# Performance work log

Hardware: AMD Instinct MI355X
Metric: run time of the kernel (lower is better)

## Reference

```python
import jax, jax.numpy as jnp
import numpy as np

D = 10          # tree depth (perfect binary tree, heap layout)
K = 2           # MAX_CHILD
N = 2 ** D - 1  # nodes per tree = 1023
LD = 256        # latent_dim
B = 128         # batch of trees


def setup_inputs() -> dict:
    key = jax.random.key(0)
    ks = jax.random.split(key, 24)
    p = lambda k, shape: (jax.random.normal(k, shape, jnp.float32) * 0.05)
    return {
        "x_embed": jax.random.normal(ks[0], (B, N, LD), jnp.float32),
        "init_embedding": jax.random.normal(ks[1], (B, LD), jnp.float32),
        # leaf gates cx, ox
        "Wcx": p(ks[2], (LD, LD)), "bcx": p(ks[3], (LD,)),
        "Wox": p(ks[4], (LD, LD)), "box": p(ks[5], (LD,)),
        # token-input gates ix, fx, ux
        "Wix": p(ks[6], (LD, LD)), "bix": p(ks[7], (LD,)),
        "Wfx": p(ks[8], (LD, LD)), "bfx": p(ks[9], (LD,)),
        "Wux": p(ks[10], (LD, LD)), "bux": p(ks[11], (LD,)),
        # per-child gates: i_gates[K], f_gates[K][K], u_gates[K]
        "Wi": p(ks[12], (K, LD, LD)), "bi": p(ks[13], (K, LD)),
        "Wf": p(ks[14], (K, K, LD, LD)), "bf": p(ks[15], (K, K, LD)),
        "Wu": p(ks[16], (K, LD, LD)), "bu": p(ks[17], (K, LD)),
        # output projection oend: Linear(3*latent_dim, latent_dim)
        "Woend": p(ks[18], (3 * LD, LD)), "boend": p(ks[19], (LD,)),
    }


def _tree_lstm(x_embed, Wcx, bcx, Wox, box, Wix, bix, Wfx, bfx, Wux, bux,
               Wi, bi, Wf, bf, Wu, bu):
    lin = lambda x, W, b: x @ W + b
    # --- leaves (deepest level): c = cx(x); h = sigmoid(ox(x)) * tanh(c) ---
    leaf_start = 2 ** (D - 1) - 1
    x_leaf = x_embed[:, leaf_start:]                       # [B, 2^(D-1), d]
    c_leaf = lin(x_leaf, Wcx, bcx)
    h_leaf = jax.nn.sigmoid(lin(x_leaf, Wox, box)) * jnp.tanh(c_leaf)
    c_all = jnp.zeros_like(x_embed).at[:, leaf_start:].set(c_leaf)
    h_all = jnp.zeros_like(x_embed).at[:, leaf_start:].set(h_leaf)
    # --- internal levels, bottom-up (fixed D-1 iterations, vectorized over B*width) ---
    for lvl in range(D - 2, -1, -1):
        s, e = 2 ** lvl - 1, 2 ** (lvl + 1) - 1
        idx = np.arange(s, e)
        ch = np.stack([2 * idx + 1, 2 * idx + 2], axis=1)  # [w, K] heap children
        hch = h_all[:, ch]                                 # [B, w, K, d]
        cch = c_all[:, ch]                                 # [B, w, K, d]
        x = x_embed[:, s:e]                                # [B, w, d]
        # i = sigmoid(ix(x) + sum_k i_gates[k](h_k))
        i = jax.nn.sigmoid(lin(x, Wix, bix)
                           + jnp.einsum('bwkd,kde->bwe', hch, Wi) + bi.sum(0))
        # f_vals[k] = fx(x) + sum_j f_gates[k][j](h_j)   (NO sigmoid, faithful to source)
        f = (lin(x, Wfx, bfx)[:, :, None, :]
             + jnp.einsum('bwjd,kjde->bwke', hch, Wf) + bf.sum(1))   # [B, w, K, d]
        # u = tanh(ux(x) + sum_k u_gates[k](h_k))
        u = jnp.tanh(lin(x, Wux, bux)
                     + jnp.einsum('bwkd,kde->bwe', hch, Wu) + bu.sum(0))
        c = i * u + jnp.sum(f * cch, axis=2)
        h = jnp.tanh(c)
        c_all = c_all.at[:, s:e].set(c)
        h_all = h_all.at[:, s:e].set(h)
    return c_all[:, 0], h_all[:, 0]                        # root state (c, h)


def reference(x_embed, init_embedding, Wcx, bcx, Wox, box, Wix, bix, Wfx, bfx,
              Wux, bux, Wi, bi, Wf, bf, Wu, bu, Woend, boend):
    c_root, h_root = _tree_lstm(x_embed, Wcx, bcx, Wox, box, Wix, bix,
                                Wfx, bfx, Wux, bux, Wi, bi, Wf, bf, Wu, bu)
    s = jnp.concatenate([init_embedding, c_root, h_root], axis=1)  # [B, 3d]
    return jnp.tanh(s @ Woend + boend)                             # [B, d]
```

## Files before the change

kernel.cpp:

```cpp
#include <hip/hip_runtime.h>
#include <hip/hip_bf16.h>
#include <math.h>


#define NNODES 1023
#define BATCH  128
#define LDIM   256

typedef __attribute__((ext_vector_type(8))) short short8;
typedef __attribute__((ext_vector_type(4))) float f32x4;

__device__ __forceinline__ float sigmoidf_(float x) {
    return 1.f / (1.f + expf(-x));
}

__device__ __forceinline__ void split3(float x, ushort& h, ushort& m, ushort& l) {
    unsigned u = __float_as_uint(x);
    unsigned hu = (u + 0x7FFFu + ((u >> 16) & 1u)) & 0xFFFF0000u;
    h = (ushort)(hu >> 16);
    float r = x - __uint_as_float(hu);
    unsigned ur = __float_as_uint(r);
    unsigned mu = (ur + 0x7FFFu + ((ur >> 16) & 1u)) & 0xFFFF0000u;
    m = (ushort)(mu >> 16);
    float r2 = r - __uint_as_float(mu);
    unsigned u2 = __float_as_uint(r2);
    l = (ushort)((u2 + 0x7FFFu + ((u2 >> 16) & 1u)) >> 16);
}

__device__ __forceinline__ unsigned cvt_pk_bf16(float lo, float hi) {
    unsigned r;
    asm("v_cvt_pk_bf16_f32 %0, %1, %2" : "=v"(r) : "v"(lo), "v"(hi));
    return r;
}

struct P3 { unsigned h, m, l; };
__device__ __forceinline__ P3 pack2v(float x0, float x1) {
    P3 p;
    p.h = cvt_pk_bf16(x0, x1);
    float h0 = __uint_as_float(p.h << 16);
    float h1 = __uint_as_float(p.h & 0xFFFF0000u);
    float r0 = x0 - h0, r1 = x1 - h1;
    p.m = cvt_pk_bf16(r0, r1);
    float m0 = __uint_as_float(p.m << 16);
    float m1 = __uint_as_float(p.m & 0xFFFF0000u);
    p.l = cvt_pk_bf16(r0 - m0, r1 - m1);
    return p;
}

struct VF { short8 h, m, l; };
__device__ __forceinline__ VF split8(float4 a, float4 b) {
    P3 p0 = pack2v(a.x, a.y), p1 = pack2v(a.z, a.w);
    P3 p2 = pack2v(b.x, b.y), p3 = pack2v(b.z, b.w);
    VF r;
    r.h = __builtin_bit_cast(short8, make_uint4(p0.h, p1.h, p2.h, p3.h));
    r.m = __builtin_bit_cast(short8, make_uint4(p0.m, p1.m, p2.m, p3.m));
    r.l = __builtin_bit_cast(short8, make_uint4(p0.l, p1.l, p2.l, p3.l));
    return r;
}

__global__ __launch_bounds__(256) void build_weights(
    const float* __restrict__ Wix, const float* __restrict__ bix,
    const float* __restrict__ Wfx, const float* __restrict__ bfx,
    const float* __restrict__ Wux, const float* __restrict__ bux,
    const float* __restrict__ Wi,  const float* __restrict__ bi,
    const float* __restrict__ Wf,  const float* __restrict__ bf,
    const float* __restrict__ Wu,  const float* __restrict__ bu,
    const float* __restrict__ Wcx, const float* __restrict__ bcx,
    const float* __restrict__ Wox, const float* __restrict__ box,
    float* __restrict__ Wbig, float* __restrict__ bias_big,
    float* __restrict__ Wleaf, float* __restrict__ bias_leaf)
{
    int i = blockIdx.x * blockDim.x + threadIdx.x;
    if (i < 768 * 1024) {
        int k = i >> 10, n = i & 1023;
        int g = n >> 8, nn = n & 255;
        float v;
        if (g == 0) {
            v = (k < 256) ? Wix[k * 256 + nn]
              : (k < 512) ? Wi[(k - 256) * 256 + nn]
                          : Wi[65536 + (k - 512) * 256 + nn];
        } else if (g == 1) {
            v = (k < 256) ? Wux[k * 256 + nn]
              : (k < 512) ? Wu[(k - 256) * 256 + nn]
                          : Wu[65536 + (k - 512) * 256 + nn];
        } else {
            int kf = g - 2;
            v = (k < 256) ? Wfx[k * 256 + nn]
              : (k < 512) ? Wf[((kf * 2 + 0) * 256 + (k - 256)) * 256 + nn]
                          : Wf[((kf * 2 + 1) * 256 + (k - 512)) * 256 + nn];
        }
        Wbig[i] = v;
        return;
    }
    i -= 768 * 1024;
    if (i < 1024) {
        int g = i >> 8, nn = i & 255;
        float v;
        if (g == 0)      v = bix[nn] + bi[nn] + bi[256 + nn];
        else if (g == 1) v = bux[nn] + bu[nn] + bu[256 + nn];
        else if (g == 2) v = bfx[nn] + bf[nn] + bf[256 + nn];
        else             v = bfx[nn] + bf[512 + nn] + bf[768 + nn];
        bias_big[i] = v;
        return;
    }
    i -= 1024;
    if (i < 256 * 512) {
        int k = i >> 9, n = i & 511;
        Wleaf[i] = (n < 256) ? Wcx[k * 256 + n] : Wox[k * 256 + (n - 256)];
        return;
    }
    i -= 256 * 512;
    if (i < 512) {
        bias_leaf[i] = (i < 256) ? bcx[i] : box[i - 256];
    }
}

__global__ __launch_bounds__(256) void split_weights_T(
    const float* __restrict__ Wbig,
    ushort* __restrict__ Wth, ushort* __restrict__ Wtm, ushort* __restrict__ Wtl)
{
    __shared__ float sh[32][33];
    const int k0 = blockIdx.x * 32, n0 = blockIdx.y * 32;
    const int t = threadIdx.x;
    {
        int r = t >> 3, c4 = (t & 7) * 4;
        float4 v = *(const float4*)&Wbig[(size_t)(k0 + r) * 1024 + n0 + c4];
        sh[r][c4] = v.x; sh[r][c4 + 1] = v.y; sh[r][c4 + 2] = v.z; sh[r][c4 + 3] = v.w;
    }
    __syncthreads();
    int n = t >> 3, kc = (t & 7) * 4;
    ushort oh[4], om[4], ol[4];
#pragma unroll
    for (int j = 0; j < 4; ++j)
        split3(sh[kc + j][n], oh[j], om[j], ol[j]);
    size_t o = (size_t)(n0 + n) * 768 + k0 + kc;
    *(ushort4*)&Wth[o] = make_ushort4(oh[0], oh[1], oh[2], oh[3]);
    *(ushort4*)&Wtm[o] = make_ushort4(om[0], om[1], om[2], om[3]);
    *(ushort4*)&Wtl[o] = make_ushort4(ol[0], ol[1], ol[2], ol[3]);
}

__global__ __launch_bounds__(256) void split_wleaf_T(
    const float* __restrict__ Wleaf,
    ushort* __restrict__ Lth, ushort* __restrict__ Ltm, ushort* __restrict__ Ltl)
{
    __shared__ float sh[32][33];
    const int k0 = blockIdx.x * 32, n0 = blockIdx.y * 32;
    const int t = threadIdx.x;
    {
        int r = t >> 3, c4 = (t & 7) * 4;
        float4 v = *(const float4*)&Wleaf[(size_t)(k0 + r) * 512 + n0 + c4];
        sh[r][c4] = v.x; sh[r][c4 + 1] = v.y; sh[r][c4 + 2] = v.z; sh[r][c4 + 3] = v.w;
    }
    __syncthreads();
    int n = t >> 3, kc = (t & 7) * 4;
    ushort oh[4], om[4], ol[4];
#pragma unroll
    for (int j = 0; j < 4; ++j)
        split3(sh[kc + j][n], oh[j], om[j], ol[j]);
    size_t o = (size_t)(n0 + n) * 256 + k0 + kc;
    *(ushort4*)&Lth[o] = make_ushort4(oh[0], oh[1], oh[2], oh[3]);
    *(ushort4*)&Ltm[o] = make_ushort4(om[0], om[1], om[2], om[3]);
    *(ushort4*)&Ltl[o] = make_ushort4(ol[0], ol[1], ol[2], ol[3]);
}

__global__ __launch_bounds__(256, 3) void mfma_level_pack(
    const float* __restrict__ x_embed,
    const float* __restrict__ hChild, const float* __restrict__ cChild,
    const ushort* __restrict__ Wth, const ushort* __restrict__ Wtm,
    const ushort* __restrict__ Wtl,
    const float* __restrict__ bias,
    float* __restrict__ hOut, float* __restrict__ cOut, int nstart)
{
    constexpr int AST = 40;
    __shared__ __align__(16) ushort Wlds[3][128 * AST];

    const int tid  = threadIdx.x;
    const int node = blockIdx.x;
    const int gy   = blockIdx.y;
    const int lane = tid & 63, wid = tid >> 6;
    const int srow = tid & 127, shalf = tid >> 7;

    const size_t nb = (size_t)(((srow >> 5) << 8) + gy * 32 + (srow & 31)) * 768;
    const ushort* w0 = Wth + nb;
    const ushort* w1 = Wtm + nb;
    const ushort* w2 = Wtl + nb;

    const int b0 = wid * 32 + (lane & 15);
    const int b1 = b0 + 16;
    const int kl = (lane >> 4) * 8;
    const float* x0p = x_embed + ((size_t)b0 * NNODES + (nstart + node)) * LDIM + kl;
    const float* x1p = x_embed + ((size_t)b1 * NNODES + (nstart + node)) * LDIM + kl;
    const float* l0p = hChild + ((size_t)(2 * node) * BATCH + b0) * LDIM + kl;
    const float* l1p = hChild + ((size_t)(2 * node) * BATCH + b1) * LDIM + kl;
    const size_t RSTEP = (size_t)BATCH * LDIM;

    f32x4 acc[8][2];
#pragma unroll
    for (int ct = 0; ct < 8; ++ct)
#pragma unroll
        for (int t2 = 0; t2 < 2; ++t2) acc[ct][t2] = (f32x4){0.f, 0.f, 0.f, 0.f};

    float4 v00, v01, v10, v11;
    int4 w00, w01, w10, w11, w20, w21;

#define TREE_LOADS(IT)                                                         \
    {                                                                          \
        const int seg_  = (IT) >> 3;                                           \
        const int koff_ = ((IT) & 7) * 32;                                     \
        const float* pa0_ = (seg_ == 0) ? x0p : (seg_ == 1) ? l0p : (l0p + RSTEP); \
        const float* pa1_ = (seg_ == 0) ? x1p : (seg_ == 1) ? l1p : (l1p + RSTEP); \
        pa0_ += koff_; pa1_ += koff_;                                          \
        v00 = *(const float4*)(pa0_);                                          \
        v01 = *(const float4*)(pa0_ + 4);                                      \
        v10 = *(const float4*)(pa1_);                                          \
        v11 = *(const float4*)(pa1_ + 4);                                      \
        const int bko_ = (IT) * 32 + shalf * 16;                               \
        w00 = *(const int4*)(w0 + bko_); w01 = *(const int4*)(w0 + bko_ + 8);  \
        w10 = *(const int4*)(w1 + bko_); w11 = *(const int4*)(w1 + bko_ + 8);  \
        w20 = *(const int4*)(w2 + bko_); w21 = *(const int4*)(w2 + bko_ + 8);  \
    }

    TREE_LOADS(0);
    for (int it = 0; it < 24; ++it) {
        if (it) __syncthreads();
        {
            const int base = srow * AST + shalf * 16;
            *(int4*)&Wlds[0][base]     = w00;
            *(int4*)&Wlds[0][base + 8] = w01;
            *(int4*)&Wlds[1][base]     = w10;
            *(int4*)&Wlds[1][base + 8] = w11;
            *(int4*)&Wlds[2][base]     = w20;
            *(int4*)&Wlds[2][base + 8] = w21;
        }
        __syncthreads();
        VF f0 = split8(v00, v01);
        VF f1 = split8(v10, v11);
        if (it + 1 < 24) TREE_LOADS(it + 1);
#pragma unroll
        for (int ct = 0; ct < 8; ++ct) {
            const int cb = (ct * 16 + (lane & 15)) * AST + (lane >> 4) * 8;
            short8 wh = *(const short8*)&Wlds[0][cb];
            short8 wm = *(const short8*)&Wlds[1][cb];
            short8 wl = *(const short8*)&Wlds[2][cb];
            acc[ct][0] = __builtin_amdgcn_mfma_f32_16x16x32_bf16(wl, f0.h, acc[ct][0], 0, 0, 0);
            acc[ct][1] = __builtin_amdgcn_mfma_f32_16x16x32_bf16(wl, f1.h, acc[ct][1], 0, 0, 0);
            acc[ct][0] = __builtin_amdgcn_mfma_f32_16x16x32_bf16(wh, f0.l, acc[ct][0], 0, 0, 0);
            acc[ct][1] = __builtin_amdgcn_mfma_f32_16x16x32_bf16(wh, f1.l, acc[ct][1], 0, 0, 0);
            acc[ct][0] = __builtin_amdgcn_mfma_f32_16x16x32_bf16(wm, f0.m, acc[ct][0], 0, 0, 0);
            acc[ct][1] = __builtin_amdgcn_mfma_f32_16x16x32_bf16(wm, f1.m, acc[ct][1], 0, 0, 0);
            acc[ct][0] = __builtin_amdgcn_mfma_f32_16x16x32_bf16(wm, f0.h, acc[ct][0], 0, 0, 0);
            acc[ct][1] = __builtin_amdgcn_mfma_f32_16x16x32_bf16(wm, f1.h, acc[ct][1], 0, 0, 0);
            acc[ct][0] = __builtin_amdgcn_mfma_f32_16x16x32_bf16(wh, f0.m, acc[ct][0], 0, 0, 0);
            acc[ct][1] = __builtin_amdgcn_mfma_f32_16x16x32_bf16(wh, f1.m, acc[ct][1], 0, 0, 0);
            acc[ct][0] = __builtin_amdgcn_mfma_f32_16x16x32_bf16(wh, f0.h, acc[ct][0], 0, 0, 0);
            acc[ct][1] = __builtin_amdgcn_mfma_f32_16x16x32_bf16(wh, f1.h, acc[ct][1], 0, 0, 0);
        }
    }
#undef TREE_LOADS

    const size_t cLb = (size_t)(2 * node) * BATCH * LDIM;
    const size_t cRb = cLb + (size_t)BATCH * LDIM;
    const size_t ob  = (size_t)node * BATCH * LDIM;
#pragma unroll
    for (int half = 0; half < 2; ++half) {
        const int nc = gy * 32 + half * 16 + ((lane >> 4) << 2);
        const float4 bi4 = *(const float4*)&bias[nc];
        const float4 bu4 = *(const float4*)&bias[256 + nc];
        const float4 b04 = *(const float4*)&bias[512 + nc];
        const float4 b14 = *(const float4*)&bias[768 + nc];
        const float bi_[4] = {bi4.x, bi4.y, bi4.z, bi4.w};
        const float bu_[4] = {bu4.x, bu4.y, bu4.z, bu4.w};
        const float b0_[4] = {b04.x, b04.y, b04.z, b04.w};
        const float b1_[4] = {b14.x, b14.y, b14.z, b14.w};
#pragma unroll
        for (int Nt = 0; Nt < 2; ++Nt) {
            const int b = wid * 32 + Nt * 16 + (lane & 15);
            float4 cL = *(const float4*)&cChild[cLb + (size_t)b * LDIM + nc];
            float4 cR = *(const float4*)&cChild[cRb + (size_t)b * LDIM + nc];
            float cl4[4] = {cL.x, cL.y, cL.z, cL.w};
            float cr4[4] = {cR.x, cR.y, cR.z, cR.w};
            float4 c4, h4;
            float* cp = (float*)&c4; float* hp = (float*)&h4;
#pragma unroll
            for (int j = 0; j < 4; ++j) {
                float gi = sigmoidf_(acc[0 + half][Nt][j] + bi_[j]);
                float gu = tanhf(acc[2 + half][Nt][j] + bu_[j]);
                float f0 = acc[4 + half][Nt][j] + b0_[j];
                float f1 = acc[6 + half][Nt][j] + b1_[j];
                float c  = gi * gu + f0 * cl4[j] + f1 * cr4[j];
                cp[j] = c;
                hp[j] = tanhf(c);
            }
            *(float4*)&cOut[ob + (size_t)b * LDIM + nc] = c4;
            *(float4*)&hOut[ob + (size_t)b * LDIM + nc] = h4;
        }
    }
}

__global__ __launch_bounds__(256, 3) void leaf_mfma(
    const float* __restrict__ x_embed,
    const ushort* __restrict__ Lth, const ushort* __restrict__ Ltm,
    const ushort* __restrict__ Ltl,
    const float* __restrict__ bias_leaf,
    float* __restrict__ hOut, float* __restrict__ cOut)
{
    constexpr int AST = 40;
    __shared__ __align__(16) ushort Wlds[3][64 * AST];
    __shared__ __align__(16) ushort Vlds[3][128 * AST];

    const int tid = threadIdx.x;
    const int ln  = blockIdx.x;
    const int gy  = blockIdx.y;
    const int lane = tid & 63, wid = tid >> 6;
    const int ni = wid & 1, bw = wid >> 1;
    const int srow = tid & 127, shalf = tid >> 7;
    const int wrow = tid & 63, whalf = (tid >> 6) & 1;

    const float* aX = x_embed + ((size_t)srow * NNODES + (511 + ln)) * LDIM;
    const size_t nbw = (size_t)(((wrow >> 5) << 8) + gy * 32 + (wrow & 31)) * 256;
    const ushort* l0 = Lth + nbw;
    const ushort* l1 = Ltm + nbw;
    const ushort* l2 = Ltl + nbw;

    f32x4 acc[2][4];
#pragma unroll
    for (int g = 0; g < 2; ++g)
#pragma unroll
        for (int t2 = 0; t2 < 4; ++t2) acc[g][t2] = (f32x4){0.f, 0.f, 0.f, 0.f};

    float4 a0, a1, a2, a3;
    int4 w00, w01, w10, w11, w20, w21;

#define LEAF_LOADS(IT)                                                         \
    {                                                                          \
        const float* ap_ = aX + (IT) * 32 + shalf * 16;                        \
        a0 = *(const float4*)(ap_);                                            \
        a1 = *(const float4*)(ap_ + 4);                                        \
        a2 = *(const float4*)(ap_ + 8);                                        \
        a3 = *(const float4*)(ap_ + 12);                                       \
        if (tid < 128) {                                                       \
            const int bko_ = (IT) * 32 + whalf * 16;                           \
            w00 = *(const int4*)(l0 + bko_); w01 = *(const int4*)(l0 + bko_ + 8); \
            w10 = *(const int4*)(l1 + bko_); w11 = *(const int4*)(l1 + bko_ + 8); \
            w20 = *(const int4*)(l2 + bko_); w21 = *(const int4*)(l2 + bko_ + 8); \
        }                                                                      \
    }

    LEAF_LOADS(0);
    for (int it = 0; it < 8; ++it) {
        if (it) __syncthreads();
        {
            P3 p0 = pack2v(a0.x, a0.y), p1 = pack2v(a0.z, a0.w);
            P3 p2 = pack2v(a1.x, a1.y), p3 = pack2v(a1.z, a1.w);
            P3 p4 = pack2v(a2.x, a2.y), p5 = pack2v(a2.z, a2.w);
            P3 p6 = pack2v(a3.x, a3.y), p7 = pack2v(a3.z, a3.w);
            const int base = srow * AST + shalf * 16;
            *(int4*)&Vlds[0][base]     = make_int4((int)p0.h, (int)p1.h, (int)p2.h, (int)p3.h);
            *(int4*)&Vlds[0][base + 8] = make_int4((int)p4.h, (int)p5.h, (int)p6.h, (int)p7.h);
            *(int4*)&Vlds[1][base]     = make_int4((int)p0.m, (int)p1.m, (int)p2.m, (int)p3.m);
            *(int4*)&Vlds[1][base + 8] = make_int4((int)p4.m, (int)p5.m, (int)p6.m, (int)p7.m);
            *(int4*)&Vlds[2][base]     = make_int4((int)p0.l, (int)p1.l, (int)p2.l, (int)p3.l);
            *(int4*)&Vlds[2][base + 8] = make_int4((int)p4.l, (int)p5.l, (int)p6.l, (int)p7.l);
            if (tid < 128) {
                const int bw_ = wrow * AST + whalf * 16;
                *(int4*)&Wlds[0][bw_]     = w00;
                *(int4*)&Wlds[0][bw_ + 8] = w01;
                *(int4*)&Wlds[1][bw_]     = w10;
                *(int4*)&Wlds[1][bw_ + 8] = w11;
                *(int4*)&Wlds[2][bw_]     = w20;
                *(int4*)&Wlds[2][bw_ + 8] = w21;
            }
        }
        __syncthreads();
        if (it + 1 < 8) LEAF_LOADS(it + 1);
        {
            short8 vf[4][3];
#pragma unroll
            for (int Nt = 0; Nt < 4; ++Nt) {
                const int rb = (bw * 64 + Nt * 16 + (lane & 15)) * AST + (lane >> 4) * 8;
#pragma unroll
                for (int s = 0; s < 3; ++s) vf[Nt][s] = *(const short8*)&Vlds[s][rb];
            }
#pragma unroll
            for (int g = 0; g < 2; ++g) {
                const int cb = (g * 32 + ni * 16 + (lane & 15)) * AST + (lane >> 4) * 8;
                short8 wh = *(const short8*)&Wlds[0][cb];
                short8 wm = *(const short8*)&Wlds[1][cb];
                short8 wl = *(const short8*)&Wlds[2][cb];
#pragma unroll
                for (int Nt = 0; Nt < 4; ++Nt)
                    acc[g][Nt] = __builtin_amdgcn_mfma_f32_16x16x32_bf16(wl, vf[Nt][0], acc[g][Nt], 0, 0, 0);
#pragma unroll
                for (int Nt = 0; Nt < 4; ++Nt)
                    acc[g][Nt] = __builtin_amdgcn_mfma_f32_16x16x32_bf16(wh, vf[Nt][2], acc[g][Nt], 0, 0, 0);
#pragma unroll
                for (int Nt = 0; Nt < 4; ++Nt)
                    acc[g][Nt] = __builtin_amdgcn_mfma_f32_16x16x32_bf16(wm, vf[Nt][1], acc[g][Nt], 0, 0, 0);
#pragma unroll
                for (int Nt = 0; Nt < 4; ++Nt)
                    acc[g][Nt] = __builtin_amdgcn_mfma_f32_16x16x32_bf16(wm, vf[Nt][0], acc[g][Nt], 0, 0, 0);
#pragma unroll
                for (int Nt = 0; Nt < 4; ++Nt)
                    acc[g][Nt] = __builtin_amdgcn_mfma_f32_16x16x32_bf16(wh, vf[Nt][1], acc[g][Nt], 0, 0, 0);
#pragma unroll
                for (int Nt = 0; Nt < 4; ++Nt)
                    acc[g][Nt] = __builtin_amdgcn_mfma_f32_16x16x32_bf16(wh, vf[Nt][0], acc[g][Nt], 0, 0, 0);
            }
        }
    }
#undef LEAF_LOADS

    const int nc = gy * 32 + ni * 16 + ((lane >> 4) << 2);
    const size_t ob = (size_t)ln * BATCH * LDIM;
    const float4 bc4 = *(const float4*)&bias_leaf[nc];
    const float4 bo4 = *(const float4*)&bias_leaf[256 + nc];
    const float bc_[4] = {bc4.x, bc4.y, bc4.z, bc4.w};
    const float bo_[4] = {bo4.x, bo4.y, bo4.z, bo4.w};
#pragma unroll
    for (int Nt = 0; Nt < 4; ++Nt) {
        const int b = bw * 64 + Nt * 16 + (lane & 15);
        float4 c4, h4;
        float* cp = (float*)&c4; float* hp = (float*)&h4;
#pragma unroll
        for (int j = 0; j < 4; ++j) {
            float c = acc[0][Nt][j] + bc_[j];
            float o = acc[1][Nt][j] + bo_[j];
            cp[j] = c;
            hp[j] = sigmoidf_(o) * tanhf(c);
        }
        size_t po = ob + (size_t)b * LDIM + nc;
        *(float4*)&cOut[po] = c4;
        *(float4*)&hOut[po] = h4;
    }
}

__global__ __launch_bounds__(256) void leaf_kernel(
    const float* __restrict__ x_embed,
    const float* __restrict__ Wleaf, const float* __restrict__ bias_leaf,
    float* __restrict__ hOut, float* __restrict__ cOut)
{
    __shared__ float As[16 * 68];
    __shared__ float Bs[2 * 16 * 64];
    float acc[2][4][4] = {};
    const int tid = threadIdx.x;
    const int ty = tid >> 4, tx = tid & 15;
    const int row0 = blockIdx.x * 64;
    const int n0 = blockIdx.y * 64;
    const int w = row0 >> 7;
    const int ar = tid >> 2;
    const int kq = (tid & 3) * 4;
    const int b = (row0 + ar) & 127;
    const float* xrow = x_embed + ((size_t)b * NNODES + 511 + w) * LDIM;

    for (int k0 = 0; k0 < 256; k0 += 16) {
        float4 av = *(const float4*)(xrow + k0 + kq);
        As[(kq + 0) * 68 + ar] = av.x;
        As[(kq + 1) * 68 + ar] = av.y;
        As[(kq + 2) * 68 + ar] = av.z;
        As[(kq + 3) * 68 + ar] = av.w;
#pragma unroll
        for (int q = 0; q < 2; ++q) {
            int L = q * 256 + tid;
            int g = L >> 8, kk = (L >> 4) & 15, n4 = (L & 15) * 4;
            float4 bv = *(const float4*)(Wleaf + (size_t)(k0 + kk) * 512 + g * 256 + n0 + n4);
            *(float4*)&Bs[(g * 16 + kk) * 64 + n4] = bv;
        }
        __syncthreads();
#pragma unroll
        for (int kk = 0; kk < 16; ++kk) {
            float4 a = *(const float4*)&As[kk * 68 + ty * 4];
            float av4[4] = {a.x, a.y, a.z, a.w};
#pragma unroll
            for (int g = 0; g < 2; ++g) {
                float4 bb = *(const float4*)&Bs[(g * 16 + kk) * 64 + tx * 4];
                float bv4[4] = {bb.x, bb.y, bb.z, bb.w};
#pragma unroll
                for (int ii = 0; ii < 4; ++ii)
#pragma unroll
                    for (int jj = 0; jj < 4; ++jj)
                        acc[g][ii][jj] += av4[ii] * bv4[jj];
            }
        }
        __syncthreads();
    }
#pragma unroll
    for (int ii = 0; ii < 4; ++ii) {
        int r = row0 + ty * 4 + ii;
        int nc = n0 + tx * 4;
        float4 c4, h4;
        float* cp = (float*)&c4; float* hp = (float*)&h4;
#pragma unroll
        for (int jj = 0; jj < 4; ++jj) {
            int n = nc + jj;
            float ac = acc[0][ii][jj] + bias_leaf[n];
            float ao = acc[1][ii][jj] + bias_leaf[256 + n];
            cp[jj] = ac;
            hp[jj] = sigmoidf_(ao) * tanhf(ac);
        }
        *(float4*)&cOut[(size_t)r * LDIM + nc] = c4;
        *(float4*)&hOut[(size_t)r * LDIM + nc] = h4;
    }
}

__global__ __launch_bounds__(256) void level_kernel(
    const float* __restrict__ x_embed,
    const float* __restrict__ hChild, const float* __restrict__ cChild,
    const float* __restrict__ Wbig, const float* __restrict__ bias_big,
    float* __restrict__ hOut, float* __restrict__ cOut,
    int nstart)
{
    __shared__ float As[16 * 68];
    __shared__ float Bs[4 * 16 * 64];
    float acc[4][4][4] = {};
    const int tid = threadIdx.x;
    const int ty = tid >> 4, tx = tid & 15;
    const int row0 = blockIdx.x * 64;
    const int n0 = blockIdx.y * 64;
    const int w = row0 >> 7;
    const int ar = tid >> 2;
    const int kq = (tid & 3) * 4;
    const int b = (row0 + ar) & 127;
    const float* srcX = x_embed + ((size_t)b * NNODES + nstart + w) * LDIM;
    const float* srcL = hChild + ((size_t)(2 * w) * BATCH + b) * LDIM;
    const float* srcR = hChild + ((size_t)(2 * w + 1) * BATCH + b) * LDIM;

    for (int k0 = 0; k0 < 768; k0 += 16) {
        int seg = k0 >> 8, off = k0 & 255;
        const float* src = (seg == 0) ? srcX : (seg == 1) ? srcL : srcR;
        float4 av = *(const float4*)(src + off + kq);
        As[(kq + 0) * 68 + ar] = av.x;
        As[(kq + 1) * 68 + ar] = av.y;
        As[(kq + 2) * 68 + ar] = av.z;
        As[(kq + 3) * 68 + ar] = av.w;
#pragma unroll
        for (int q = 0; q < 4; ++q) {
            int L = q * 256 + tid;
            int g = L >> 8, kk = (L >> 4) & 15, n4 = (L & 15) * 4;
            float4 bv = *(const float4*)(Wbig + (size_t)(k0 + kk) * 1024 + g * 256 + n0 + n4);
            *(float4*)&Bs[(g * 16 + kk) * 64 + n4] = bv;
        }
        __syncthreads();
#pragma unroll
        for (int kk = 0; kk < 16; ++kk) {
            float4 a = *(const float4*)&As[kk * 68 + ty * 4];
            float av4[4] = {a.x, a.y, a.z, a.w};
#pragma unroll
            for (int g = 0; g < 4; ++g) {
                float4 bb = *(const float4*)&Bs[(g * 16 + kk) * 64 + tx * 4];
                float bv4[4] = {bb.x, bb.y, bb.z, bb.w};
#pragma unroll
                for (int ii = 0; ii < 4; ++ii)
#pragma unroll
                    for (int jj = 0; jj < 4; ++jj)
                        acc[g][ii][jj] += av4[ii] * bv4[jj];
            }
        }
        __syncthreads();
    }
    const size_t cLbase = ((size_t)(2 * w) * BATCH) * LDIM;
    const size_t cRbase = ((size_t)(2 * w + 1) * BATCH) * LDIM;
#pragma unroll
    for (int ii = 0; ii < 4; ++ii) {
        int r = row0 + ty * 4 + ii;
        int bb2 = r & 127;
        int nc = n0 + tx * 4;
        float4 cL = *(const float4*)&cChild[cLbase + (size_t)bb2 * LDIM + nc];
        float4 cR = *(const float4*)&cChild[cRbase + (size_t)bb2 * LDIM + nc];
        float cl4[4] = {cL.x, cL.y, cL.z, cL.w};
        float cr4[4] = {cR.x, cR.y, cR.z, cR.w};
        float4 c4, h4;
        float* cp = (float*)&c4; float* hp = (float*)&h4;
#pragma unroll
        for (int jj = 0; jj < 4; ++jj) {
            int n = nc + jj;
            float gi = sigmoidf_(acc[0][ii][jj] + bias_big[n]);
            float gu = tanhf(acc[1][ii][jj] + bias_big[256 + n]);
            float f0 = acc[2][ii][jj] + bias_big[512 + n];
            float f1 = acc[3][ii][jj] + bias_big[768 + n];
            float c = gi * gu + f0 * cl4[jj] + f1 * cr4[jj];
            cp[jj] = c;
            hp[jj] = tanhf(c);
        }
        *(float4*)&cOut[(size_t)r * LDIM + nc] = c4;
        *(float4*)&hOut[(size_t)r * LDIM + nc] = h4;
    }
}

__global__ __launch_bounds__(256) void gemm_part4(
    const float* __restrict__ x_embed, const float* __restrict__ hChild,
    const float* __restrict__ Wbig,
    float* __restrict__ part, int nstart, int rowsTotal)
{
    __shared__ float As[16 * 68];
    __shared__ float Bs[4 * 16 * 64];
    float acc[4][4][4] = {};
    const int tid = threadIdx.x;
    const int ty = tid >> 4, tx = tid & 15;
    const int row0 = blockIdx.x * 64;
    const int n0 = blockIdx.y * 64;
    const int seg = blockIdx.z;
    const int w = row0 >> 7;
    const int ar = tid >> 2;
    const int kq = (tid & 3) * 4;
    const int b = (row0 + ar) & 127;
    const float* src =
        (seg == 0) ? x_embed + ((size_t)b * NNODES + nstart + w) * LDIM
                   : hChild + ((size_t)(2 * w + (seg - 1)) * BATCH + b) * LDIM;

    for (int k0 = 0; k0 < 256; k0 += 16) {
        float4 av = *(const float4*)(src + k0 + kq);
        As[(kq + 0) * 68 + ar] = av.x;
        As[(kq + 1) * 68 + ar] = av.y;
        As[(kq + 2) * 68 + ar] = av.z;
        As[(kq + 3) * 68 + ar] = av.w;
#pragma unroll
        for (int q = 0; q < 4; ++q) {
            int L = q * 256 + tid;
            int g = L >> 8, kk = (L >> 4) & 15, n4 = (L & 15) * 4;
            float4 bv = *(const float4*)(Wbig + (size_t)(seg * 256 + k0 + kk) * 1024
                                         + g * 256 + n0 + n4);
            *(float4*)&Bs[(g * 16 + kk) * 64 + n4] = bv;
        }
        __syncthreads();
#pragma unroll
        for (int kk = 0; kk < 16; ++kk) {
            float4 a = *(const float4*)&As[kk * 68 + ty * 4];
            float av4[4] = {a.x, a.y, a.z, a.w};
#pragma unroll
            for (int g = 0; g < 4; ++g) {
                float4 bb = *(const float4*)&Bs[(g * 16 + kk) * 64 + tx * 4];
                float bv4[4] = {bb.x, bb.y, bb.z, bb.w};
#pragma unroll
                for (int ii = 0; ii < 4; ++ii)
#pragma unroll
                    for (int jj = 0; jj < 4; ++jj)
                        acc[g][ii][jj] += av4[ii] * bv4[jj];
            }
        }
        __syncthreads();
    }
#pragma unroll
    for (int ii = 0; ii < 4; ++ii) {
        int r = row0 + ty * 4 + ii;
        size_t base = ((size_t)seg * rowsTotal + r) * 1024 + n0 + tx * 4;
#pragma unroll
        for (int g = 0; g < 4; ++g)
            *(float4*)&part[base + g * 256] = *(float4*)acc[g][ii];
    }
}

__global__ __launch_bounds__(256) void combine_eps(
    const float* __restrict__ part, const float* __restrict__ cChild,
    const float* __restrict__ bias,
    float* __restrict__ hOut, float* __restrict__ cOut, int rowsTotal)
{
    int idx = blockIdx.x * 256 + threadIdx.x;
    int row = idx >> 6, n = (idx & 63) * 4;
    size_t sseg = (size_t)rowsTotal * 1024;
    const float* p0 = part + (size_t)row * 1024 + n;
    float s[4][4];
#pragma unroll
    for (int g = 0; g < 4; ++g) {
        float4 a = *(const float4*)(p0 + g * 256);
        float4 b = *(const float4*)(p0 + sseg + g * 256);
        float4 c = *(const float4*)(p0 + 2 * sseg + g * 256);
        s[g][0] = a.x + b.x + c.x; s[g][1] = a.y + b.y + c.y;
        s[g][2] = a.z + b.z + c.z; s[g][3] = a.w + b.w + c.w;
    }
    int node = row >> 7, b = row & 127;
    float4 cL = *(const float4*)&cChild[((size_t)(2 * node) * BATCH + b) * LDIM + n];
    float4 cR = *(const float4*)&cChild[((size_t)(2 * node + 1) * BATCH + b) * LDIM + n];
    float cl4[4] = {cL.x, cL.y, cL.z, cL.w};
    float cr4[4] = {cR.x, cR.y, cR.z, cR.w};
    float4 c4, h4;
    float* cp = (float*)&c4; float* hp = (float*)&h4;
#pragma unroll
    for (int jj = 0; jj < 4; ++jj) {
        int nn = n + jj;
        float gi = sigmoidf_(s[0][jj] + bias[nn]);
        float gu = tanhf(s[1][jj] + bias[256 + nn]);
        float f0 = s[2][jj] + bias[512 + nn];
        float f1 = s[3][jj] + bias[768 + nn];
        float c = gi * gu + f0 * cl4[jj] + f1 * cr4[jj];
        cp[jj] = c;
        hp[jj] = tanhf(c);
    }
    *(float4*)&cOut[(size_t)row * LDIM + n] = c4;
    *(float4*)&hOut[(size_t)row * LDIM + n] = h4;
}

__global__ __launch_bounds__(256) void final_kernel(
    const float* __restrict__ init_emb,
    const float* __restrict__ cRoot, const float* __restrict__ hRoot,
    const float* __restrict__ Woend, const float* __restrict__ boend,
    float* __restrict__ out)
{
    __shared__ float sv[768];
    int b = blockIdx.x, t = threadIdx.x;
    sv[t]       = init_emb[(size_t)b * 256 + t];
    sv[256 + t] = cRoot[(size_t)b * 256 + t];
    sv[512 + t] = hRoot[(size_t)b * 256 + t];
    __syncthreads();
    float acc = boend[t];
#pragma unroll 4
    for (int d = 0; d < 768; ++d)
        acc += sv[d] * Woend[(size_t)d * 256 + t];
    out[(size_t)b * 256 + t] = tanhf(acc);
}

extern "C" void kernel_launch(void* const* d_in, const int* in_sizes, int n_in,
                              void* d_out, int out_size, void* d_ws, size_t ws_size,
                              hipStream_t stream)
{
    const float* x_embed  = (const float*)d_in[0];
    const float* init_emb = (const float*)d_in[1];
    const float* Wcx = (const float*)d_in[2];  const float* bcx = (const float*)d_in[3];
    const float* Wox = (const float*)d_in[4];  const float* box = (const float*)d_in[5];
    const float* Wix = (const float*)d_in[6];  const float* bix = (const float*)d_in[7];
    const float* Wfx = (const float*)d_in[8];  const float* bfx = (const float*)d_in[9];
    const float* Wux = (const float*)d_in[10]; const float* bux = (const float*)d_in[11];
    const float* Wi  = (const float*)d_in[12]; const float* bi  = (const float*)d_in[13];
    const float* Wf  = (const float*)d_in[14]; const float* bf  = (const float*)d_in[15];
    const float* Wu  = (const float*)d_in[16]; const float* bu  = (const float*)d_in[17];
    const float* Woend = (const float*)d_in[18]; const float* boend = (const float*)d_in[19];
    float* out = (float*)d_out;
    float* ws  = (float*)d_ws;

    size_t off = 0;
    float* hA = ws + off; off += (size_t)512 * 128 * 256;
    float* cA = ws + off; off += (size_t)512 * 128 * 256;
    float* hB = ws + off; off += (size_t)256 * 128 * 256;
    float* cB = ws + off; off += (size_t)256 * 128 * 256;
    float* Wbig      = ws + off; off += (size_t)768 * 1024;
    float* bias_big  = ws + off; off += 1024;
    float* Wleaf     = ws + off; off += (size_t)256 * 512;
    float* bias_leaf = ws + off; off += 512;
    ushort* Wth = (ushort*)(ws + off); off += (size_t)768 * 1024 / 2;
    ushort* Wtm = (ushort*)(ws + off); off += (size_t)768 * 1024 / 2;
    ushort* Wtl = (ushort*)(ws + off); off += (size_t)768 * 1024 / 2;
    ushort* Lth = (ushort*)(ws + off); off += (size_t)512 * 256 / 2;
    ushort* Ltm = (ushort*)(ws + off); off += (size_t)512 * 256 / 2;
    ushort* Ltl = (ushort*)(ws + off); off += (size_t)512 * 256 / 2;
    size_t mfma_need = off * sizeof(float);
    size_t part_off = off;
    float* part = ws + part_off;

    bool mfma_ok = mfma_need <= ws_size;

    {
        int total = 768 * 1024 + 1024 + 256 * 512 + 512;
        int blocks = (total + 255) / 256;
        build_weights<<<blocks, 256, 0, stream>>>(
            Wix, bix, Wfx, bfx, Wux, bux, Wi, bi, Wf, bf, Wu, bu,
            Wcx, bcx, Wox, box, Wbig, bias_big, Wleaf, bias_leaf);
    }
    if (mfma_ok) {
        split_weights_T<<<dim3(24, 32), 256, 0, stream>>>(Wbig, Wth, Wtm, Wtl);
        split_wleaf_T<<<dim3(8, 16), 256, 0, stream>>>(Wleaf, Lth, Ltm, Ltl);
    }

    if (mfma_ok) {
        leaf_mfma<<<dim3(512, 8), 256, 0, stream>>>(
            x_embed, Lth, Ltm, Ltl, bias_leaf, hA, cA);
    } else {
        leaf_kernel<<<dim3(1024, 4), 256, 0, stream>>>(
            x_embed, Wleaf, bias_leaf, hA, cA);
    }

    float* hbufs[2] = {hA, hB};
    float* cbufs[2] = {cA, cB};
    int child = 0;
    for (int lvl = 8; lvl >= 0; --lvl) {
        int W = 1 << lvl, s = W - 1;
        int outb = child ^ 1;
        size_t rows = (size_t)W * 128;
        bool split = (W <= 16) &&
                     ((part_off + 3 * rows * 1024) * sizeof(float) <= ws_size);
        if (lvl >= 5 && mfma_ok) {
            mfma_level_pack<<<dim3(W, 8), 256, 0, stream>>>(
                x_embed, hbufs[child], cbufs[child], Wth, Wtm, Wtl, bias_big,
                hbufs[outb], cbufs[outb], s);
        } else if (split) {
            gemm_part4<<<dim3(W * 2, 4, 3), 256, 0, stream>>>(
                x_embed, hbufs[child], Wbig, part, s, (int)rows);
            combine_eps<<<(int)(rows / 4), 256, 0, stream>>>(
                part, cbufs[child], bias_big, hbufs[outb], cbufs[outb], (int)rows);
        } else {
            level_kernel<<<dim3(W * 2, 4), 256, 0, stream>>>(
                x_embed, hbufs[child], cbufs[child], Wbig, bias_big,
                hbufs[outb], cbufs[outb], s);
        }
        child = outb;
    }

    final_kernel<<<128, 256, 0, stream>>>(init_emb, cbufs[child], hbufs[child],
                                          Woend, boend, out);
}
```

Baseline: 1.080 ms.

## Double-buffer weight tiles in LDS with conflict-free layout and MFMA priority

Weight tiles for the level kernel now go into two LDS buffers, so the next tile's store overlaps the current MFMA loop. This cuts the two barriers per iteration to one. Global weight loads are issued two iterations ahead, and the LDS layout is reorganised to a k-chunk-major form with no padding. s_setprio is raised around the MFMA block. The cost is more LDS per block (48KB vs 30KB), which may reduce occupancy below the launch-bounds target of 3 blocks, plus more live registers from the deeper prefetch.

Measured after the change: 1.064 ms (median of 2 runs). Within noise of the previous version (-1.4%).

```diff
diff --git a/kernel.cpp b/kernel.cpp
--- a/kernel.cpp
+++ b/kernel.cpp
@@ -171,8 +171,7 @@
     const float* __restrict__ bias,
     float* __restrict__ hOut, float* __restrict__ cOut, int nstart)
 {
-    constexpr int AST = 40;
-    __shared__ __align__(16) ushort Wlds[3][128 * AST];
+    __shared__ __align__(16) ushort Wlds[2][12288];
 
     const int tid  = threadIdx.x;
     const int node = blockIdx.x;
@@ -194,6 +193,9 @@
     const float* l1p = hChild + ((size_t)(2 * node) * BATCH + b1) * LDIM + kl;
     const size_t RSTEP = (size_t)BATCH * LDIM;
 
+    const int wbase = 2 * shalf * 1024 + srow * 8;
+    const int rbase = (lane >> 4) * 1024 + (lane & 15) * 8;
+
     f32x4 acc[8][2];
 #pragma unroll
     for (int ct = 0; ct < 8; ++ct)
@@ -203,7 +205,14 @@
     float4 v00, v01, v10, v11;
     int4 w00, w01, w10, w11, w20, w21;
 
-#define TREE_LOADS(IT)                                                         \
+#define W_LOADS(IT)                                                            \
+    {                                                                          \
+        const int bko_ = (IT) * 32 + shalf * 16;                               \
+        w00 = *(const int4*)(w0 + bko_); w01 = *(const int4*)(w0 + bko_ + 8);  \
+        w10 = *(const int4*)(w1 + bko_); w11 = *(const int4*)(w1 + bko_ + 8);  \
+        w20 = *(const int4*)(w2 + bko_); w21 = *(const int4*)(w2 + bko_ + 8);  \
+    }
+#define ACT_LOADS(IT)                                                          \
     {                                                                          \
         const int seg_  = (IT) >> 3;                                           \
         const int koff_ = ((IT) & 7) * 32;                                     \
@@ -214,34 +223,34 @@
         v01 = *(const float4*)(pa0_ + 4);                                      \
         v10 = *(const float4*)(pa1_);                                          \
         v11 = *(const float4*)(pa1_ + 4);                                      \
-        const int bko_ = (IT) * 32 + shalf * 16;                               \
-        w00 = *(const int4*)(w0 + bko_); w01 = *(const int4*)(w0 + bko_ + 8);  \
-        w10 = *(const int4*)(w1 + bko_); w11 = *(const int4*)(w1 + bko_ + 8);  \
-        w20 = *(const int4*)(w2 + bko_); w21 = *(const int4*)(w2 + bko_ + 8);  \
-    }
-
-    TREE_LOADS(0);
+    }
+#define WRITE_W(BUF)                                                           \
+    {                                                                          \
+        ushort* wp_ = &Wlds[BUF][wbase];                                       \
+        *(int4*)(wp_)        = w00; *(int4*)(wp_ + 1024) = w01;                \
+        *(int4*)(wp_ + 4096) = w10; *(int4*)(wp_ + 5120) = w11;                \
+        *(int4*)(wp_ + 8192) = w20; *(int4*)(wp_ + 9216) = w21;                \
+    }
+
+    W_LOADS(0); ACT_LOADS(0);
+    WRITE_W(0);
+    W_LOADS(1);
+    __syncthreads();
+
     for (int it = 0; it < 24; ++it) {
-        if (it) __syncthreads();
-        {
-            const int base = srow * AST + shalf * 16;
-            *(int4*)&Wlds[0][base]     = w00;
-            *(int4*)&Wlds[0][base + 8] = w01;
-            *(int4*)&Wlds[1][base]     = w10;
-            *(int4*)&Wlds[1][base + 8] = w11;
-            *(int4*)&Wlds[2][base]     = w20;
-            *(int4*)&Wlds[2][base + 8] = w21;
-        }
-        __syncthreads();
+        const int cur = it & 1;
+        if (it + 1 < 24) WRITE_W(cur ^ 1);
+        if (it + 2 < 24) W_LOADS(it + 2);
         VF f0 = split8(v00, v01);
         VF f1 = split8(v10, v11);
-        if (it + 1 < 24) TREE_LOADS(it + 1);
+        if (it + 1 < 24) ACT_LOADS(it + 1);
+        const ushort* lb = &Wlds[cur][rbase];
+        __builtin_amdgcn_s_setprio(1);
 #pragma unroll
         for (int ct = 0; ct < 8; ++ct) {
-            const int cb = (ct * 16 + (lane & 15)) * AST + (lane >> 4) * 8;
-            short8 wh = *(const short8*)&Wlds[0][cb];
-            short8 wm = *(const short8*)&Wlds[1][cb];
-            short8 wl = *(const short8*)&Wlds[2][cb];
+            short8 wh = *(const short8*)(lb + ct * 128);
+            short8 wm = *(const short8*)(lb + 4096 + ct * 128);
+            short8 wl = *(const short8*)(lb + 8192 + ct * 128);
             acc[ct][0] = __builtin_amdgcn_mfma_f32_16x16x32_bf16(wl, f0.h, acc[ct][0], 0, 0, 0);
             acc[ct][1] = __builtin_amdgcn_mfma_f32_16x16x32_bf16(wl, f1.h, acc[ct][1], 0, 0, 0);
             acc[ct][0] = __builtin_amdgcn_mfma_f32_16x16x32_bf16(wh, f0.l, acc[ct][0], 0, 0, 0);
@@ -255,8 +264,12 @@
             acc[ct][0] = __builtin_amdgcn_mfma_f32_16x16x32_bf16(wh, f0.h, acc[ct][0], 0, 0, 0);
             acc[ct][1] = __builtin_amdgcn_mfma_f32_16x16x32_bf16(wh, f1.h, acc[ct][1], 0, 0, 0);
         }
-    }
-#undef TREE_LOADS
+        __builtin_amdgcn_s_setprio(0);
+        __syncthreads();
+    }
+#undef W_LOADS
+#undef ACT_LOADS
+#undef WRITE_W
 
     const size_t cLb = (size_t)(2 * node) * BATCH * LDIM;
     const size_t cRb = cLb + (size_t)BATCH * LDIM;
```
